# Performance work log

Hardware: AMD Instinct MI355X
Metric: run time of the kernel (lower is better)

Reference implementation:

```python
import jax, jax.numpy as jnp
import numpy as np

H = 128   # d_model / features
N = 32    # kept complex modes (d_state=64 -> 32 conjugate pairs)
B = 8
L = 8192


def setup_inputs() -> dict:
    key = jax.random.key(0)
    ks = jax.random.split(key, 8)
    x = jax.random.normal(ks[0], (B, H, L), jnp.float32)
    # S4D (diagonal SSM) kernel parameters; channels=2 for bidirectional
    C_re = (jax.random.normal(ks[1], (2, H, N), jnp.float32) * (0.5 ** 0.5))
    C_im = (jax.random.normal(ks[2], (2, H, N), jnp.float32) * (0.5 ** 0.5))
    log_A_real = jnp.log(0.5 * jnp.ones((H, N), jnp.float32))          # S4D-Lin init
    A_imag = jnp.tile(np.pi * jnp.arange(N, dtype=jnp.float32), (H, 1))
    # log_dt uniform in [log(1e-3), log(1e-1)]
    u = jax.random.uniform(ks[3], (H,), jnp.float32)
    log_dt = u * (np.log(0.1) - np.log(0.001)) + np.log(0.001)
    D = jax.random.normal(ks[4], (H,), jnp.float32)                    # skip term
    W_pw = jax.random.normal(ks[5], (H, H), jnp.float32) / np.sqrt(H)  # 1x1 conv weight (out, in)
    gamma = jnp.ones((H,), jnp.float32)
    beta = jnp.zeros((H,), jnp.float32)
    return {"x": x, "C_re": C_re, "C_im": C_im, "log_A_real": log_A_real,
            "A_imag": A_imag, "log_dt": log_dt, "D": D, "W_pw": W_pw,
            "gamma": gamma, "beta": beta}


def reference(x, C_re, C_im, log_A_real, A_imag, log_dt, D, W_pw, gamma, beta):
    Lx = x.shape[-1]
    # ---- S4D SSM kernel via Vandermonde (ZOH discretization) ----
    A = -jnp.exp(log_A_real) + 1j * A_imag                 # (H, N) complex
    dt = jnp.exp(log_dt)[:, None]                          # (H, 1)
    dtA = A * dt                                           # (H, N)
    C = C_re + 1j * C_im                                   # (2, H, N)
    Kc = C * ((jnp.exp(dtA) - 1.0) / A)                    # (2, H, N)
    vand = jnp.exp(dtA[:, :, None] * jnp.arange(Lx))       # (H, N, L)
    k = 2.0 * jnp.einsum('chn,hnl->chl', Kc, vand).real    # (2, H, L)
    # ---- bidirectional: causal half + anticausal (flipped) half ----
    k_full = (jnp.pad(k[0], ((0, 0), (0, Lx)))
              + jnp.pad(k[1][:, ::-1], ((0, 0), (Lx, 0))))  # (H, 2L)
    # ---- FFT convolution ----
    n = 2 * Lx
    y = jnp.fft.irfft(jnp.fft.rfft(x, n=n) * jnp.fft.rfft(k_full, n=n), n=n)[..., :Lx]
    y = y + x * D[:, None]                                 # skip connection
    y = jax.nn.gelu(y, approximate=False)                  # FFTConv default activation
    # ---- pointwise 1x1 conv (no bias) ----
    y = jnp.einsum('bhl,oh->bol', y, W_pw)
    # ---- BatchNorm1d (training-mode batch statistics) ----
    mean = jnp.mean(y, axis=(0, 2), keepdims=True)
    var = jnp.var(y, axis=(0, 2), keepdims=True)
    y = (y - mean) * jax.lax.rsqrt(var + 1e-5) * gamma[:, None] + beta[:, None]
    # ---- ELU + residual (dropout p=0) ----
    return jax.nn.elu(y) + x
```

## Files before the change

### kernel.cpp

```cpp
#include <hip/hip_runtime.h>
#include <math.h>

#define HCH   128
#define NMODE 32
#define BB    8
#define LLEN  8192
#define LC    256
#define CCH   (LLEN / LC)
#define ROWS  (BB * HCH)

typedef unsigned int uint;
typedef _Float16 f16x8 __attribute__((ext_vector_type(8)));
typedef float    f32x4 __attribute__((ext_vector_type(4)));

static __device__ __forceinline__ uint pk2(float a, float b) {
    union { _Float16 h[2]; uint u; } v;
    v.h[0] = (_Float16)a; v.h[1] = (_Float16)b;
    return v.u;
}

__device__ __forceinline__ float gelu_f(float y) {
    float z = fabsf(y) * 0.7071067811865476f;
    float p = fmaf(z, 0.078108f, 0.000972f);
    p = fmaf(z, p, 0.230389f);
    p = fmaf(z, p, 0.278393f);
    p = fmaf(z, p, 1.0f);
    float p2 = p * p;
    float p4 = p2 * p2;
    float er = 1.f - __builtin_amdgcn_rcpf(p4);
    float s  = copysignf(er, y);
    return 0.5f * y * (1.f + s);
}

#define DPP_ADD(v, ctrl) { int _t = __builtin_amdgcn_update_dpp(0, __float_as_int(v), \
                             (ctrl), 0xF, 0xF, true); (v) += __int_as_float(_t); }

__global__ __launch_bounds__(256) void k_prep(const float* __restrict__ C_re,
                                              const float* __restrict__ C_im,
                                              const float* __restrict__ logA,
                                              const float* __restrict__ Aim,
                                              const float* __restrict__ logdt,
                                              const float* __restrict__ W,
                                              _Float16* __restrict__ cT,
                                              uint* __restrict__ kmg,
                                              _Float16* __restrict__ eT,
                                              _Float16* __restrict__ Wh,
                                              float* __restrict__ Pw,
                                              float* __restrict__ stats) {
    __shared__ float2 PL[32 * 257];
    __shared__ float4 G01[32];
    __shared__ float4 HG[32];
    __shared__ float2 WL[32];
    __shared__ float k0L[256], k1L[256];
    __shared__ _Float16 KMl[516];
    int tid  = threadIdx.x;
    int h    = blockIdx.x >> 1;
    int half = blockIdx.x & 1;
    if (blockIdx.x == 0) stats[tid] = 0.f;
    if (half == 0 && tid < 128) Wh[h * 128 + tid] = (_Float16)W[h * 128 + tid];
    if (tid < 32) {
        int n = tid, idx = h * 32 + n;
        float ar = expf(logA[idx]);
        float ai = Aim[idx];
        float dt = expf(logdt[h]);
        float dre = -ar * dt, dim = ai * dt;
        float er = expf(dre);
        float wr = er * cosf(dim), wi = er * sinf(dim);
        WL[n] = (float2){wr, wi};
        if (half == 0) {
            float eL = expf(dre * 256.f);
            Pw[idx]        = eL * cosf(dim * 256.f);
            Pw[4096 + idx] = eL * sinf(dim * 256.f);
        }
        float den  = ar * ar + ai * ai;
        float numr = -(wr - 1.f) * ar + wi * ai;
        float numi = -wi * ar - (wr - 1.f) * ai;
        float Kr = numr / den, Ki = numi / den;
        float c0r = C_re[idx],        c0i = C_im[idx];
        float c1r = C_re[4096 + idx], c1i = C_im[4096 + idx];
        float g0r = 2.f * (c0r * Kr - c0i * Ki), g0i = 2.f * (c0r * Ki + c0i * Kr);
        float g1r = 2.f * (c1r * Kr - c1i * Ki);
        float g1i = 2.f * (c1r * Ki + c1i * Kr);
        G01[n] = (float4){g0r, g0i, g1r, g1i};
        HG[n]  = (float4){g0r * wr - g0i * wi, g0r * wi + g0i * wr, g1r, g1i};
    }
    __syncthreads();
    {
        int n = tid & 31, tg = tid >> 5;
        float2 w = WL[n];
        float w2r = w.x * w.x - w.y * w.y,   w2i = 2.f * w.x * w.y;
        float w4r = w2r * w2r - w2i * w2i,   w4i = 2.f * w2r * w2i;
        float w8r = w4r * w4r - w4i * w4i,   w8i = 2.f * w4r * w4i;
        float pr = (tg & 1) ? w.x : 1.f;
        float pi = (tg & 1) ? w.y : 0.f;
        if (tg & 2) { float t2 = pr * w2r - pi * w2i; pi = pr * w2i + pi * w2r; pr = t2; }
        if (tg & 4) { float t4 = pr * w4r - pi * w4i; pi = pr * w4i + pi * w4r; pr = t4; }
        float2* row = &PL[n * 257];
        #pragma unroll
        for (int j = 0; j < 32; j++) {
            row[tg + 8 * j] = (float2){pr, pi};
            float tr = pr * w8r - pi * w8i; pi = pr * w8i + pi * w8r; pr = tr;
        }
    }
    __syncthreads();
    {
        int tau = tid;
        float s0 = 0.f, s1 = 0.f;
        #pragma unroll
        for (int n = 0; n < 32; n++) {
            float2 p = PL[n * 257 + tau];
            float4 g = G01[n];
            s0 += g.x * p.x - g.y * p.y;
            s1 += g.z * p.x - g.w * p.y;
        }
        k0L[tau] = s0; k1L[tau] = s1;
    }
    __syncthreads();
    if (half == 0) {
        KMl[tid]       = (_Float16)k0L[255 - tid];
        KMl[256 + tid] = (_Float16)k1L[tid];
        if (tid == 0) { KMl[512] = (_Float16)0.f; KMl[513] = (_Float16)0.f; }
    }
    __syncthreads();
    if (half == 0) {
        union { _Float16 hh[2]; uint u; } pa, pb;
        pa.hh[0] = KMl[2 * tid];     pa.hh[1] = KMl[2 * tid + 1];
        pb.hh[0] = KMl[2 * tid + 1]; pb.hh[1] = KMl[2 * tid + 2];
        kmg[(size_t)h * 512 + tid]       = pa.u;
        kmg[(size_t)h * 512 + 256 + tid] = pb.u;
    }
    #pragma unroll 4
    for (int i = 0; i < 16; i++) {
        int idx = i * 256 + tid;
        int n = idx & 31;
        int t = half * 128 + (idx >> 5);
        float2 pt = PL[n * 257 + t];
        float2 pu = PL[n * 257 + 255 - t];
        float4 hg = HG[n];
        size_t rb = ((size_t)(h * 256 + t)) * 128;
        *(uint*)&cT[rb + 2 * n]      = pk2(hg.x * pt.x - hg.y * pt.y,
                                           -(hg.x * pt.y + hg.y * pt.x));
        *(uint*)&cT[rb + 64 + 2 * n] = pk2(hg.z * pu.x - hg.w * pu.y,
                                           -(hg.z * pu.y + hg.w * pu.x));
    }
    #pragma unroll 4
    for (int i = 0; i < 16; i++) {
        int idx = i * 256 + tid;
        int n = idx >> 7;
        int s = half * 128 + (idx & 127);
        float2 ps = PL[n * 257 + s];
        float2 pu = PL[n * 257 + 255 - s];
        size_t base = (size_t)h * 128 * 256;
        eT[base + (size_t)(2 * n) * 256 + s]      = (_Float16)pu.x;
        eT[base + (size_t)(2 * n + 1) * 256 + s]  = (_Float16)pu.y;
        eT[base + (size_t)(64 + 2 * n) * 256 + s] = (_Float16)ps.x;
        eT[base + (size_t)(65 + 2 * n) * 256 + s] = (_Float16)ps.y;
    }
}

__global__ __launch_bounds__(256, 2) void k_states_c(const float* __restrict__ x,
                                                     const _Float16* __restrict__ eT,
                                                     const float* __restrict__ Pw,
                                                     _Float16* __restrict__ xh,
                                                     _Float16* __restrict__ carr) {
    __shared__ float Sf[128 * 66];
    _Float16* SMh = (_Float16*)Sf;
    int tid = threadIdx.x;
    int xcd = blockIdx.x & 7, slot = blockIdx.x >> 3;
    int h = xcd * 16 + (slot >> 2);
    int mt = (slot >> 1) & 1, d = slot & 1;
    int wave = tid >> 6, lane = tid & 63;
    int wm = wave >> 1, wn = wave & 1;
    int lrow = lane & 15, quad = lane >> 4;
    int koff = quad * 8;
    f32x4 acc[4][2];
    #pragma unroll
    for (int a = 0; a < 4; a++)
        #pragma unroll
        for (int b = 0; b < 2; b++) acc[a][b] = (f32x4){0.f, 0.f, 0.f, 0.f};

    const int chA = tid >> 3, segA = tid & 7;
    const size_t xbase = (((size_t)(mt * 4) * HCH + h) << 13) + (chA << 8) + segA * 4;
    const int rB = tid >> 2, sgB = tid & 3;

    float4 ar[4]; uint4 br;
    #define LOADA_S(kk) { _Pragma("unroll") for (int i = 0; i < 4; i++) \
        ar[i] = *(const float4*)(x + xbase + ((size_t)i << 20) + (kk)); }
    #define LOADB_S(kk) { br = *(const uint4*)(eT + ((size_t)(h * 128 + d * 64 + rB)) * 256 + (kk) + sgB * 8); }
    #define WRITE_S(buf, kk) { _Pragma("unroll") for (int i = 0; i < 4; i++) { \
            uint2 o; o.x = pk2(ar[i].x, ar[i].y); o.y = pk2(ar[i].z, ar[i].w); \
            *(uint2*)&SMh[(buf) * 5120 + (chA + 32 * i) * 40 + segA * 4] = o; \
            if (d == 0) *(uint2*)&xh[xbase + ((size_t)i << 20) + (kk)] = o; } \
        *(uint4*)&SMh[10240 + (buf) * 2560 + rB * 40 + sgB * 8] = br; }

    LOADA_S(0); LOADB_S(0);
    WRITE_S(0, 0);
    __syncthreads();
    for (int kt = 0; kt < 8; kt++) {
        int cur = kt & 1;
        if (kt < 7) { LOADA_S((kt + 1) * 32); LOADB_S((kt + 1) * 32); }
        f16x8 a[4], b[2];
        #pragma unroll
        for (int f = 0; f < 4; f++)
            a[f] = *(const f16x8*)&SMh[cur * 5120 + (wm * 64 + f * 16 + lrow) * 40 + koff];
        #pragma unroll
        for (int f = 0; f < 2; f++)
            b[f] = *(const f16x8*)&SMh[10240 + cur * 2560 + (wn * 32 + f * 16 + lrow) * 40 + koff];
        #pragma unroll
        for (int fi = 0; fi < 4; fi++)
            #pragma unroll
            for (int fj = 0; fj < 2; fj++)
                acc[fi][fj] = __builtin_amdgcn_mfma_f32_16x16x32_f16(a[fi], b[fj], acc[fi][fj], 0, 0, 0);
        if (kt < 7) {
            WRITE_S(cur ^ 1, (kt + 1) * 32);
            __syncthreads();
        }
    }
    __syncthreads();
    #pragma unroll
    for (int fi = 0; fi < 4; fi++) {
        #pragma unroll
        for (int fj = 0; fj < 2; fj++) {
            int srow = wn * 32 + fj * 16 + lrow;
            #pragma unroll
            for (int rg = 0; rg < 4; rg++) {
                int bc = wm * 64 + fi * 16 + quad * 4 + rg;
                Sf[bc * 66 + srow] = acc[fi][fj][rg];
            }
        }
    }
    __syncthreads();
    if (tid < 128) {
        int bloc = tid >> 5, n = tid & 31;
        float wLr = Pw[h * 32 + n], wLi = Pw[4096 + h * 32 + n];
        float cr = 0.f, ci = 0.f;
        size_t gb = ((size_t)(h * 256 + mt * 128 + bloc * 32)) * 128 + d * 64 + 2 * n;
        if (d == 0) {
            for (int c = 0; c < CCH; c++) {
                *(uint*)&carr[gb + (size_t)c * 128] = pk2(cr, ci);
                float2 s = *(const float2*)&Sf[(bloc * 32 + c) * 66 + 2 * n];
                float nr = fmaf(wLr, cr, -wLi * ci) + s.x;
                float ni = fmaf(wLi, cr,  wLr * ci) + s.y;
                cr = nr; ci = ni;
            }
        } else {
            for (int c = CCH - 1; c >= 0; c--) {
                *(uint*)&carr[gb + (size_t)c * 128] = pk2(cr, ci);
                float2 s = *(const float2*)&Sf[(bloc * 32 + c) * 66 + 2 * n];
                float nr = fmaf(wLr, cr, -wLi * ci) + s.x;
                float ni = fmaf(wLi, cr,  wLr * ci) + s.y;
                cr = nr; ci = ni;
            }
        }
    }
    #undef LOADA_S
    #undef LOADB_S
    #undef WRITE_S
}

__global__ __launch_bounds__(256, 4) void k_conv_g(const _Float16* __restrict__ xh,
                                                   const uint* __restrict__ kmg,
                                                   const _Float16* __restrict__ cT,
                                                   const _Float16* __restrict__ carr,
                                                   const float* __restrict__ D,
                                                   _Float16* __restrict__ Yg) {
    __shared__ _Float16 At[2][128 * 40];
    __shared__ _Float16 Bc[64 * 128];
    __shared__ uint KMA[256], KMB[256];
    int tid = threadIdx.x;
    int xcd = blockIdx.x & 7, slot = blockIdx.x >> 3;
    int h   = xcd * 16 + (slot >> 3);
    int sub = slot & 7;
    int mt = sub >> 2, nt = sub & 3;
    int wave = tid >> 6, lane = tid & 63;
    int wm = wave >> 1, wn = wave & 1;
    int lrow = lane & 15, quad = lane >> 4;
    int koff = quad * 8;
    f32x4 acc[4][2];
    #pragma unroll
    for (int a = 0; a < 4; a++)
        #pragma unroll
        for (int b = 0; b < 2; b++) acc[a][b] = (f32x4){0.f, 0.f, 0.f, 0.f};

    const int rS = tid >> 2, sgS = tid & 3;

    uint4 a_r[2];
    #define LOADA_C(kk) { _Pragma("unroll") for (int i = 0; i < 2; i++) { \
            int bc = mt * 128 + rS + 64 * i; \
            a_r[i] = ((kk) < 256) \
              ? *(const uint4*)(xh + (((size_t)((bc >> 5) * HCH + h)) << 13) + ((bc & 31) << 8) + (kk) + sgS * 8) \
              : *(const uint4*)(carr + ((size_t)(h * 256 + bc)) * 128 + ((kk) - 256) + sgS * 8); } }
    #define WRITE_A(buf) { _Pragma("unroll") for (int i = 0; i < 2; i++) \
        *(uint4*)&At[buf][(rS + 64 * i) * 40 + sgS * 8] = a_r[i]; }

    KMA[tid] = kmg[(size_t)h * 512 + tid];
    KMB[tid] = kmg[(size_t)h * 512 + 256 + tid];
    #pragma unroll
    for (int i = 0; i < 4; i++) {
        int idx = tid + i * 256;
        int r = idx >> 4, sg = idx & 15;
        uint4 v = *(const uint4*)(cT + ((size_t)(h * 256 + nt * 64 + r)) * 128 + sg * 8);
        *(uint4*)&Bc[r * 128 + ((sg * 8) ^ ((r & 7) << 3))] = v;
    }
    LOADA_C(0);
    WRITE_A(0);
    __syncthreads();
    for (int kt = 0; kt < 12; kt++) {
        int cur = kt & 1;
        if (kt < 11) LOADA_C((kt + 1) * 32);
        f16x8 a[4], b[2];
        #pragma unroll
        for (int f = 0; f < 4; f++)
            a[f] = *(const f16x8*)&At[cur][(wm * 64 + f * 16 + lrow) * 40 + koff];
        if (kt < 8) {
            int kk = kt * 32;
            #pragma unroll
            for (int f = 0; f < 2; f++) {
                int t_f = nt * 64 + wn * 32 + f * 16 + lrow;
                int idx0 = 255 - t_f + kk + koff;
                int par = idx0 & 1;
                int dw = idx0 >> 1;
                const uint* kp = par ? KMB : KMA;
                union { uint u[4]; f16x8 v; } bu;
                bu.u[0] = kp[dw]; bu.u[1] = kp[dw + 1]; bu.u[2] = kp[dw + 2]; bu.u[3] = kp[dw + 3];
                b[f] = bu.v;
            }
        } else {
            int cb = kt * 32 - 256 + koff;
            #pragma unroll
            for (int f = 0; f < 2; f++) {
                int r2 = wn * 32 + f * 16 + lrow;
                b[f] = *(const f16x8*)&Bc[r2 * 128 + (cb ^ ((r2 & 7) << 3))];
            }
        }
        #pragma unroll
        for (int fi = 0; fi < 4; fi++)
            #pragma unroll
            for (int fj = 0; fj < 2; fj++)
                acc[fi][fj] = __builtin_amdgcn_mfma_f32_16x16x32_f16(a[fi], b[fj], acc[fi][fj], 0, 0, 0);
        if (kt < 11) {
            WRITE_A(cur ^ 1);
            __syncthreads();
        }
    }
    float Dh = D[h];
    #pragma unroll
    for (int fi = 0; fi < 4; fi++) {
        #pragma unroll
        for (int fj = 0; fj < 2; fj++) {
            int t = nt * 64 + wn * 32 + fj * 16 + lrow;
            #pragma unroll
            for (int rg = 0; rg < 4; rg++) {
                int bc = mt * 128 + wm * 64 + fi * 16 + quad * 4 + rg;
                size_t base = (((size_t)((bc >> 5) * HCH + h)) << 13) + ((bc & 31) << 8) + t;
                float xv = (float)xh[base];
                float yv = acc[fi][fj][rg] + Dh * xv;
                Yg[base] = (_Float16)gelu_f(yv);
            }
        }
    }
    #undef LOADA_C
    #undef WRITE_A
}

__global__ __launch_bounds__(256, 2) void k_pointwise(const _Float16* __restrict__ Yg,
                                                      const _Float16* __restrict__ Wh,
                                                      _Float16* __restrict__ z,
                                                      float* __restrict__ stats) {
    __shared__ _Float16 Yt[2][128 * 40];
    __shared__ float Ls[512];
    int tid = threadIdx.x;
    int b  = blockIdx.x >> 6;
    int l0 = (blockIdx.x & 63) << 7;
    int wave = tid >> 6, lane = tid & 63;
    int wm = wave >> 1, wn = wave & 1;
    int lrow = lane & 15, quad = lane >> 4;
    int koff = quad * 8;
    f32x4 acc[4][4];
    #pragma unroll
    for (int a = 0; a < 4; a++)
        #pragma unroll
        for (int c = 0; c < 4; c++) acc[a][c] = (f32x4){0.f, 0.f, 0.f, 0.f};

    f16x8 a[4][4];
    #pragma unroll
    for (int ks = 0; ks < 4; ks++)
        #pragma unroll
        for (int f = 0; f < 4; f++)
            a[ks][f] = *(const f16x8*)(Wh + (wm * 64 + f * 16 + lrow) * HCH + ks * 32 + koff);

    const int hhS = tid & 31;
    const int lgbase = tid >> 5;
    uint4 yv[2];
    #define LOADY(kk) { _Pragma("unroll") for (int i = 0; i < 2; i++) \
        yv[i] = *(const uint4*)(Yg + (((size_t)(b * HCH + (kk) + hhS)) << 13) + l0 + (lgbase + 8 * i) * 8); }
    #define WRITEY(buf) { _Pragma("unroll") for (int i = 0; i < 2; i++) { \
            const _Float16* hv = (const _Float16*)&yv[i]; \
            _Pragma("unroll") for (int j = 0; j < 8; j++) \
                Yt[buf][((lgbase + 8 * i) * 8 + j) * 40 + hhS] = hv[j]; } }

    LOADY(0);
    WRITEY(0);
    __syncthreads();
    for (int kt = 0; kt < 4; kt++) {
        int cur = kt & 1;
        if (kt < 3) LOADY((kt + 1) * 32);
        f16x8 bf[4];
        #pragma unroll
        for (int f = 0; f < 4; f++)
            bf[f] = *(const f16x8*)&Yt[cur][(wn * 64 + f * 16 + lrow) * 40 + koff];
        #pragma unroll
        for (int fi = 0; fi < 4; fi++)
            #pragma unroll
            for (int fj = 0; fj < 4; fj++)
                acc[fi][fj] = __builtin_amdgcn_mfma_f32_16x16x32_f16(a[kt][fi], bf[fj], acc[fi][fj], 0, 0, 0);
        if (kt < 3) {
            WRITEY(cur ^ 1);
            __syncthreads();
        }
    }
    #pragma unroll
    for (int fi = 0; fi < 4; fi++) {
        #pragma unroll
        for (int fj = 0; fj < 4; fj++) {
            int l = l0 + wn * 64 + fj * 16 + lrow;
            #pragma unroll
            for (int rg = 0; rg < 4; rg++) {
                int o = wm * 64 + fi * 16 + quad * 4 + rg;
                z[(((size_t)(b * HCH + o)) << 13) + l] = (_Float16)acc[fi][fj][rg];
            }
        }
    }
    #pragma unroll
    for (int fi = 0; fi < 4; fi++) {
        #pragma unroll
        for (int rg = 0; rg < 4; rg++) {
            float s = 0.f, q = 0.f;
            #pragma unroll
            for (int fj = 0; fj < 4; fj++) {
                float v = acc[fi][fj][rg];
                s += v; q = fmaf(v, v, q);
            }
            DPP_ADD(s, 0xB1); DPP_ADD(s, 0x4E); DPP_ADD(s, 0x141); DPP_ADD(s, 0x140);
            DPP_ADD(q, 0xB1); DPP_ADD(q, 0x4E); DPP_ADD(q, 0x141); DPP_ADD(q, 0x140);
            if (lrow == 0) {
                int olo = fi * 16 + quad * 4 + rg;
                Ls[wave * 64 + olo]       = s;
                Ls[256 + wave * 64 + olo] = q;
            }
        }
    }
    __syncthreads();
    if (tid < HCH) {
        int wmn = tid >> 6;
        int olo = tid & 63;
        float s = Ls[(wmn * 2) * 64 + olo] + Ls[(wmn * 2 + 1) * 64 + olo];
        float q = Ls[256 + (wmn * 2) * 64 + olo] + Ls[256 + (wmn * 2 + 1) * 64 + olo];
        atomicAdd(&stats[tid], s);
        atomicAdd(&stats[HCH + tid], q);
    }
    #undef LOADY
    #undef WRITEY
}

__global__ __launch_bounds__(256) void k_final(const _Float16* __restrict__ z,
                                               const _Float16* __restrict__ xh,
                                               const float* __restrict__ stats,
                                               const float* __restrict__ gamma,
                                               const float* __restrict__ beta,
                                               float* __restrict__ out) {
    size_t i8 = (size_t)blockIdx.x * 256 + threadIdx.x;
    int o = (int)((i8 >> 10) & (HCH - 1));
    const float inv_cnt = 1.f / (float)(BB * LLEN);
    float m   = stats[o] * inv_cnt;
    float var = stats[HCH + o] * inv_cnt - m * m;
    float rs  = rsqrtf(var + 1e-5f);
    float ga  = gamma[o] * rs;
    float bt  = beta[o] - m * ga;
    uint4 zv = ((const uint4*)z)[i8];
    uint4 xv = ((const uint4*)xh)[i8];
    const _Float16* zh = (const _Float16*)&zv;
    const _Float16* xf = (const _Float16*)&xv;
    float4 ra, rb;
    { float t = fmaf((float)zh[0], ga, bt); float e = t > 0.f ? t : (__expf(t) - 1.f); ra.x = e + (float)xf[0]; }
    { float t = fmaf((float)zh[1], ga, bt); float e = t > 0.f ? t : (__expf(t) - 1.f); ra.y = e + (float)xf[1]; }
    { float t = fmaf((float)zh[2], ga, bt); float e = t > 0.f ? t : (__expf(t) - 1.f); ra.z = e + (float)xf[2]; }
    { float t = fmaf((float)zh[3], ga, bt); float e = t > 0.f ? t : (__expf(t) - 1.f); ra.w = e + (float)xf[3]; }
    { float t = fmaf((float)zh[4], ga, bt); float e = t > 0.f ? t : (__expf(t) - 1.f); rb.x = e + (float)xf[4]; }
    { float t = fmaf((float)zh[5], ga, bt); float e = t > 0.f ? t : (__expf(t) - 1.f); rb.y = e + (float)xf[5]; }
    { float t = fmaf((float)zh[6], ga, bt); float e = t > 0.f ? t : (__expf(t) - 1.f); rb.z = e + (float)xf[6]; }
    { float t = fmaf((float)zh[7], ga, bt); float e = t > 0.f ? t : (__expf(t) - 1.f); rb.w = e + (float)xf[7]; }
    ((float4*)out)[2 * i8]     = ra;
    ((float4*)out)[2 * i8 + 1] = rb;
}

extern "C" void kernel_launch(void* const* d_in, const int* in_sizes, int n_in,
                              void* d_out, int out_size, void* d_ws, size_t ws_size,
                              hipStream_t stream) {
    const float* x     = (const float*)d_in[0];
    const float* C_re  = (const float*)d_in[1];
    const float* C_im  = (const float*)d_in[2];
    const float* logA  = (const float*)d_in[3];
    const float* Aim   = (const float*)d_in[4];
    const float* logdt = (const float*)d_in[5];
    const float* D     = (const float*)d_in[6];
    const float* W     = (const float*)d_in[7];
    const float* gamma = (const float*)d_in[8];
    const float* beta  = (const float*)d_in[9];

    float* ws = (float*)d_ws;
    _Float16* eT    = (_Float16*)ws;
    _Float16* Yg    = (_Float16*)ws;
    _Float16* zf    = (_Float16*)(ws + 8388608);
    _Float16* cT    = (_Float16*)(ws + 12582912);
    uint*     kmg   = (uint*)(ws + 14680064);
    _Float16* carr  = (_Float16*)(ws + 16777216);
    float*    Pw    = ws + 16777216 + 2097152;
    float*    stats = Pw + 8192;
    _Float16* Wh    = (_Float16*)(ws + 18882880);
    _Float16* xh    = (_Float16*)(ws + 18891072);
    float*    out   = (float*)d_out;

    k_prep     <<<256,  256, 0, stream>>>(C_re, C_im, logA, Aim, logdt, W, cT, kmg, eT, Wh, Pw, stats);
    k_states_c <<<512,  256, 0, stream>>>(x, eT, Pw, xh, carr);
    k_conv_g   <<<1024, 256, 0, stream>>>(xh, kmg, cT, carr, D, Yg);
    k_pointwise<<<512,  256, 0, stream>>>(Yg, Wh, zf, stats);
    k_final    <<<4096, 256, 0, stream>>>(zf, xh, stats, gamma, beta, out);
}
```

Baseline: 173.3 us.

## Deepen register prefetch to two stages and load full Y tile up front

In the state and convolution kernels, global loads are now issued two K-steps ahead using a pair of register staging buffers, which gives more latency hiding between load and use. In the pointwise kernel, the double-buffered K loop with per-step syncs is replaced by one bulk load of the whole 128x128 Y tile into a single padded shared buffer. That removes three barriers and lets all global loads be in flight at once. The cost is higher register pressure (more staging registers) and a larger shared footprint in the pointwise kernel, which may reduce occupancy.

```diff
diff --git a/kernel.cpp b/kernel.cpp
--- a/kernel.cpp
+++ b/kernel.cpp
@@ -183,22 +183,23 @@
     const size_t xbase = (((size_t)(mt * 4) * HCH + h) << 13) + (chA << 8) + segA * 4;
     const int rB = tid >> 2, sgB = tid & 3;
 
-    float4 ar[4]; uint4 br;
-    #define LOADA_S(kk) { _Pragma("unroll") for (int i = 0; i < 4; i++) \
-        ar[i] = *(const float4*)(x + xbase + ((size_t)i << 20) + (kk)); }
-    #define LOADB_S(kk) { br = *(const uint4*)(eT + ((size_t)(h * 128 + d * 64 + rB)) * 256 + (kk) + sgB * 8); }
-    #define WRITE_S(buf, kk) { _Pragma("unroll") for (int i = 0; i < 4; i++) { \
-            uint2 o; o.x = pk2(ar[i].x, ar[i].y); o.y = pk2(ar[i].z, ar[i].w); \
+    float4 ar[2][4]; uint4 br[2];
+    #define LOADA_S(s, kk) { _Pragma("unroll") for (int i = 0; i < 4; i++) \
+        ar[s][i] = *(const float4*)(x + xbase + ((size_t)i << 20) + (kk)); }
+    #define LOADB_S(s, kk) { br[s] = *(const uint4*)(eT + ((size_t)(h * 128 + d * 64 + rB)) * 256 + (kk) + sgB * 8); }
+    #define WRITE_S(s, buf, kk) { _Pragma("unroll") for (int i = 0; i < 4; i++) { \
+            uint2 o; o.x = pk2(ar[s][i].x, ar[s][i].y); o.y = pk2(ar[s][i].z, ar[s][i].w); \
             *(uint2*)&SMh[(buf) * 5120 + (chA + 32 * i) * 40 + segA * 4] = o; \
             if (d == 0) *(uint2*)&xh[xbase + ((size_t)i << 20) + (kk)] = o; } \
-        *(uint4*)&SMh[10240 + (buf) * 2560 + rB * 40 + sgB * 8] = br; }
-
-    LOADA_S(0); LOADB_S(0);
-    WRITE_S(0, 0);
+        *(uint4*)&SMh[10240 + (buf) * 2560 + rB * 40 + sgB * 8] = br[s]; }
+
+    LOADA_S(0, 0);  LOADB_S(0, 0);
+    LOADA_S(1, 32); LOADB_S(1, 32);
+    WRITE_S(0, 0, 0);
     __syncthreads();
     for (int kt = 0; kt < 8; kt++) {
         int cur = kt & 1;
-        if (kt < 7) { LOADA_S((kt + 1) * 32); LOADB_S((kt + 1) * 32); }
+        if (kt < 6) { LOADA_S(kt & 1, (kt + 2) * 32); LOADB_S(kt & 1, (kt + 2) * 32); }
         f16x8 a[4], b[2];
         #pragma unroll
         for (int f = 0; f < 4; f++)
@@ -212,7 +213,7 @@
             for (int fj = 0; fj < 2; fj++)
                 acc[fi][fj] = __builtin_amdgcn_mfma_f32_16x16x32_f16(a[fi], b[fj], acc[fi][fj], 0, 0, 0);
         if (kt < 7) {
-            WRITE_S(cur ^ 1, (kt + 1) * 32);
+            WRITE_S((kt + 1) & 1, cur ^ 1, (kt + 1) * 32);
             __syncthreads();
         }
     }
@@ -284,15 +285,17 @@
 
     const int rS = tid >> 2, sgS = tid & 3;
 
-    uint4 a_r[2];
-    #define LOADA_C(kk) { _Pragma("unroll") for (int i = 0; i < 2; i++) { \
+    uint4 a_r[2][2];
+    #define LOADA_C(s, kk) { _Pragma("unroll") for (int i = 0; i < 2; i++) { \
             int bc = mt * 128 + rS + 64 * i; \
-            a_r[i] = ((kk) < 256) \
+            a_r[s][i] = ((kk) < 256) \
               ? *(const uint4*)(xh + (((size_t)((bc >> 5) * HCH + h)) << 13) + ((bc & 31) << 8) + (kk) + sgS * 8) \
               : *(const uint4*)(carr + ((size_t)(h * 256 + bc)) * 128 + ((kk) - 256) + sgS * 8); } }
-    #define WRITE_A(buf) { _Pragma("unroll") for (int i = 0; i < 2; i++) \
-        *(uint4*)&At[buf][(rS + 64 * i) * 40 + sgS * 8] = a_r[i]; }
-
+    #define WRITE_A(s, buf) { _Pragma("unroll") for (int i = 0; i < 2; i++) \
+        *(uint4*)&At[buf][(rS + 64 * i) * 40 + sgS * 8] = a_r[s][i]; }
+
+    LOADA_C(0, 0);
+    LOADA_C(1, 32);
     KMA[tid] = kmg[(size_t)h * 512 + tid];
     KMB[tid] = kmg[(size_t)h * 512 + 256 + tid];
     #pragma unroll
@@ -302,12 +305,11 @@
         uint4 v = *(const uint4*)(cT + ((size_t)(h * 256 + nt * 64 + r)) * 128 + sg * 8);
         *(uint4*)&Bc[r * 128 + ((sg * 8) ^ ((r & 7) << 3))] = v;
     }
-    LOADA_C(0);
-    WRITE_A(0);
+    WRITE_A(0, 0);
     __syncthreads();
     for (int kt = 0; kt < 12; kt++) {
         int cur = kt & 1;
-        if (kt < 11) LOADA_C((kt + 1) * 32);
+        if (kt < 10) LOADA_C(kt & 1, (kt + 2) * 32);
         f16x8 a[4], b[2];
         #pragma unroll
         for (int f = 0; f < 4; f++)
@@ -339,7 +341,7 @@
             for (int fj = 0; fj < 2; fj++)
                 acc[fi][fj] = __builtin_amdgcn_mfma_f32_16x16x32_f16(a[fi], b[fj], acc[fi][fj], 0, 0, 0);
         if (kt < 11) {
-            WRITE_A(cur ^ 1);
+            WRITE_A((kt + 1) & 1, cur ^ 1);
             __syncthreads();
         }
     }
@@ -367,7 +369,7 @@
                                                       const _Float16* __restrict__ Wh,
                                                       _Float16* __restrict__ z,
                                                       float* __restrict__ stats) {
-    __shared__ _Float16 Yt[2][128 * 40];
+    __shared__ _Float16 Yt[128 * 136];
     __shared__ float Ls[512];
     int tid = threadIdx.x;
     int b  = blockIdx.x >> 6;
@@ -382,42 +384,40 @@
         #pragma unroll
         for (int c = 0; c < 4; c++) acc[a][c] = (f32x4){0.f, 0.f, 0.f, 0.f};
 
+    uint4 yv[8];
+    #pragma unroll
+    for (int i = 0; i < 8; i++) {
+        int g = i * 256 + tid;
+        int hh = g >> 4, lg = g & 15;
+        yv[i] = *(const uint4*)(Yg + (((size_t)(b * HCH + hh)) << 13) + l0 + lg * 8);
+    }
     f16x8 a[4][4];
     #pragma unroll
     for (int ks = 0; ks < 4; ks++)
         #pragma unroll
         for (int f = 0; f < 4; f++)
             a[ks][f] = *(const f16x8*)(Wh + (wm * 64 + f * 16 + lrow) * HCH + ks * 32 + koff);
-
-    const int hhS = tid & 31;
-    const int lgbase = tid >> 5;
-    uint4 yv[2];
-    #define LOADY(kk) { _Pragma("unroll") for (int i = 0; i < 2; i++) \
-        yv[i] = *(const uint4*)(Yg + (((size_t)(b * HCH + (kk) + hhS)) << 13) + l0 + (lgbase + 8 * i) * 8); }
-    #define WRITEY(buf) { _Pragma("unroll") for (int i = 0; i < 2; i++) { \
-            const _Float16* hv = (const _Float16*)&yv[i]; \
-            _Pragma("unroll") for (int j = 0; j < 8; j++) \
-                Yt[buf][((lgbase + 8 * i) * 8 + j) * 40 + hhS] = hv[j]; } }
-
-    LOADY(0);
-    WRITEY(0);
-    __syncthreads();
+    #pragma unroll
+    for (int i = 0; i < 8; i++) {
+        int g = i * 256 + tid;
+        int hh = g >> 4, lg = g & 15;
+        const _Float16* hv = (const _Float16*)&yv[i];
+        #pragma unroll
+        for (int j = 0; j < 8; j++)
+            Yt[(lg * 8 + j) * 136 + hh] = hv[j];
+    }
+    __syncthreads();
+    #pragma unroll
     for (int kt = 0; kt < 4; kt++) {
-        int cur = kt & 1;
-        if (kt < 3) LOADY((kt + 1) * 32);
         f16x8 bf[4];
         #pragma unroll
         for (int f = 0; f < 4; f++)
-            bf[f] = *(const f16x8*)&Yt[cur][(wn * 64 + f * 16 + lrow) * 40 + koff];
+            bf[f] = *(const f16x8*)&Yt[(wn * 64 + f * 16 + lrow) * 136 + kt * 32 + koff];
         #pragma unroll
         for (int fi = 0; fi < 4; fi++)
             #pragma unroll
             for (int fj = 0; fj < 4; fj++)
                 acc[fi][fj] = __builtin_amdgcn_mfma_f32_16x16x32_f16(a[kt][fi], bf[fj], acc[fi][fj], 0, 0, 0);
-        if (kt < 3) {
-            WRITEY(cur ^ 1);
-            __syncthreads();
-        }
     }
     #pragma unroll
     for (int fi = 0; fi < 4; fi++) {
@@ -459,8 +459,6 @@
         atomicAdd(&stats[tid], s);
         atomicAdd(&stats[HCH + tid], q);
     }
-    #undef LOADY
-    #undef WRITEY
 }
 
 __global__ __launch_bounds__(256) void k_final(const _Float16* __restrict__ z,
```

New measurement: 209.7 us. 1.21x slower.
